# Optimization experiments

Measured on AMD Instinct MI355X. Metric: run time of the kernel, lower is better.

Reference implementation:

```python
import jax, jax.numpy as jnp
import numpy as np

B, T, I, H, O = 64, 1024, 64, 512, 24


def _gru_cell(x, h, w_ih, w_hh, b_ih, b_hh):
    # PyTorch GRUCell math. w_ih: [3H, in], w_hh: [3H, H]
    gi = x @ w_ih.T + b_ih   # [B, 3H]
    gh = h @ w_hh.T + b_hh   # [B, 3H]
    i_r, i_z, i_n = jnp.split(gi, 3, axis=-1)
    h_r, h_z, h_n = jnp.split(gh, 3, axis=-1)
    r = jax.nn.sigmoid(i_r + h_r)
    z = jax.nn.sigmoid(i_z + h_z)
    n = jnp.tanh(i_n + r * h_n)
    return (1.0 - z) * n + z * h


def setup_inputs() -> dict:
    key = jax.random.key(0)
    ks = jax.random.split(key, 13)
    s1 = 1.0 / np.sqrt(H)
    u = lambda k, shape: jax.random.uniform(k, shape, jnp.float32, -s1, s1)
    return {
        "x": jax.random.normal(ks[0], (B, T, I), jnp.float32),
        "w_ih1": u(ks[1], (3 * H, I)),
        "w_hh1": u(ks[2], (3 * H, H)),
        "b_ih1": u(ks[3], (3 * H,)),
        "b_hh1": u(ks[4], (3 * H,)),
        "w_ih2": u(ks[5], (3 * H, H)),
        "w_hh2": u(ks[6], (3 * H, H)),
        "b_ih2": u(ks[7], (3 * H,)),
        "b_hh2": u(ks[8], (3 * H,)),
        "w_o1": u(ks[9], (O, H)),
        "b_o1": u(ks[10], (O,)),
        "w_o2": u(ks[11], (O, H)),
        "b_o2": u(ks[12], (O,)),
    }


def reference(x, w_ih1, w_hh1, b_ih1, b_hh1, w_ih2, w_hh2, b_ih2, b_hh2,
              w_o1, b_o1, w_o2, b_o2):
    batch = x.shape[0]
    h0 = jnp.zeros((batch, H), x.dtype)

    def step(carry, x_t):
        h1, h2 = carry
        h1 = _gru_cell(x_t, h1, w_ih1, w_hh1, b_ih1, b_hh1)
        h2 = _gru_cell(h1, h2, w_ih2, w_hh2, b_ih2, b_hh2)
        out = jnp.tanh(h1 @ w_o1.T + b_o1) + jnp.tanh(h2 @ w_o2.T + b_o2)
        return (h1, h2), out

    xs = jnp.transpose(x, (1, 0, 2))  # [T, B, I]
    _, outs = jax.lax.scan(step, (h0, h0), xs)  # outs: [T, B, O]
    return jnp.transpose(outs, (1, 0, 2))  # [B, T, O]
```

## Files before the change

kernel.cpp:

```cpp
#include <hip/hip_runtime.h>

typedef unsigned short u16;
typedef unsigned int u32;
typedef unsigned long long u64;
typedef __attribute__((ext_vector_type(8))) short bf16x8;
typedef __attribute__((ext_vector_type(4))) float f32x4;
typedef __attribute__((ext_vector_type(4))) u32 u32x4;

namespace {
constexpr int kT = 1024, kI = 64, kH = 512, kO = 24;
constexpr int kBH = 64 * kH;
constexpr int kNWG = 100;
constexpr unsigned kBarOff = 16u * (unsigned)kBH * 2u;
}

__device__ __forceinline__ u16 f2bf(float f) {
  union { float f; u32 u; } c; c.f = f;
  u32 u = c.u + 0x7FFFu + ((c.u >> 16) & 1u);
  return (u16)(u >> 16);
}
__device__ __forceinline__ float sigf(float x) { return 1.0f / (1.0f + __expf(-x)); }
__device__ __forceinline__ float tanhf_(float x) {
  float e = __expf(2.0f * x); return 1.0f - 2.0f / (e + 1.0f);
}
__device__ __forceinline__ bf16x8 cvt8(const float* p) {
  const float4 f0 = *reinterpret_cast<const float4*>(p);
  const float4 f1 = *reinterpret_cast<const float4*>(p + 4);
  bf16x8 r;
  r[0] = (short)f2bf(f0.x); r[1] = (short)f2bf(f0.y);
  r[2] = (short)f2bf(f0.z); r[3] = (short)f2bf(f0.w);
  r[4] = (short)f2bf(f1.x); r[5] = (short)f2bf(f1.y);
  r[6] = (short)f2bf(f1.z); r[7] = (short)f2bf(f1.w);
  return r;
}
__device__ __forceinline__ f32x4 mfma(bf16x8 a, bf16x8 b, f32x4 c) {
  return __builtin_amdgcn_mfma_f32_16x16x32_bf16(a, b, c, 0, 0, 0);
}
__device__ __forceinline__ int ldflag(const int* s, int i) {
  return __hip_atomic_load(&s[i], __ATOMIC_RELAXED, __HIP_MEMORY_SCOPE_AGENT);
}
__device__ __forceinline__ void stflag(int* s, int i, int v) {
  __hip_atomic_store(&s[i], v, __ATOMIC_RELAXED, __HIP_MEMORY_SCOPE_AGENT);
}
__device__ __forceinline__ void barrier_lds() {
  asm volatile("s_waitcnt lgkmcnt(0)" ::: "memory");
  __builtin_amdgcn_s_barrier();
}
union V16 { u32x4 u; bf16x8 v; };
__device__ __forceinline__ void fetch4(const u16* p, bf16x8* ch) {
  u32x4 a, b, c, d;
  asm volatile(
    "global_load_dwordx4 %0, %4, off sc0 sc1\n\t"
    "global_load_dwordx4 %1, %4, off offset:64 sc0 sc1\n\t"
    "global_load_dwordx4 %2, %4, off offset:128 sc0 sc1\n\t"
    "global_load_dwordx4 %3, %4, off offset:192 sc0 sc1\n\t"
    "s_waitcnt vmcnt(0)"
    : "=&v"(a), "=&v"(b), "=&v"(c), "=&v"(d) : "v"(p) : "memory");
  V16 t;
  t.u = a; ch[0] = t.v;  t.u = b; ch[1] = t.v;
  t.u = c; ch[2] = t.v;  t.u = d; ch[3] = t.v;
}
__device__ __forceinline__ void fetch8(const u16* p, bf16x8* ch) {
  u32x4 a, b, c, d, e, f, g2, h;
  asm volatile(
    "global_load_dwordx4 %0, %8, off sc0 sc1\n\t"
    "global_load_dwordx4 %1, %8, off offset:64 sc0 sc1\n\t"
    "global_load_dwordx4 %2, %8, off offset:128 sc0 sc1\n\t"
    "global_load_dwordx4 %3, %8, off offset:192 sc0 sc1\n\t"
    "global_load_dwordx4 %4, %8, off offset:256 sc0 sc1\n\t"
    "global_load_dwordx4 %5, %8, off offset:320 sc0 sc1\n\t"
    "global_load_dwordx4 %6, %8, off offset:384 sc0 sc1\n\t"
    "global_load_dwordx4 %7, %8, off offset:448 sc0 sc1\n\t"
    "s_waitcnt vmcnt(0)"
    : "=&v"(a), "=&v"(b), "=&v"(c), "=&v"(d),
      "=&v"(e), "=&v"(f), "=&v"(g2), "=&v"(h) : "v"(p) : "memory");
  V16 t;
  t.u = a; ch[0] = t.v;  t.u = b;  ch[1] = t.v;
  t.u = c; ch[2] = t.v;  t.u = d;  ch[3] = t.v;
  t.u = e; ch[4] = t.v;  t.u = f;  ch[5] = t.v;
  t.u = g2; ch[6] = t.v; t.u = h;  ch[7] = t.v;
}
__device__ __forceinline__ u32 pat3(int t3) {
  return ((u32)t3 & 1u) | ((((u32)t3 >> 1) & 1u) << 16);
}
template<int N>
__device__ __forceinline__ bool tagsok(const bf16x8* ch, u32 pat) {
  bool ok = true;
#pragma unroll
  for (int c = 0; c < N; ++c) {
    union { bf16x8 v; u32 u[4]; } t; t.v = ch[c];
    ok = ok && ((t.u[0] & 0x10001u) == pat) && ((t.u[2] & 0x10001u) == pat);
  }
  return ok;
}
template<int N>
__device__ __forceinline__ void dataD(const u16* p, u32 pat, bf16x8* ch) {
  int spins = 0;
  for (;;) {
    u64 g0 = __hip_atomic_load((const u64*)p, __ATOMIC_RELAXED, __HIP_MEMORY_SCOPE_AGENT);
    if (__all(((u32)g0 & 0x10001u) == pat)) break;
    if ((++spins & 3) == 3) __builtin_amdgcn_s_sleep(1);
  }
  spins = 0;
  for (;;) {
    if constexpr (N == 4) fetch4(p, ch); else fetch8(p, ch);
    if (__all(tagsok<N>(ch, pat))) break;
    if ((++spins & 7) == 7) __builtin_amdgcn_s_sleep(1);
  }
  __asm__ volatile("" ::: "memory");
}
template<int N>
__device__ __forceinline__ void dataO(const u16* p, u32 pat, bf16x8* ch) {
  if constexpr (N == 4) fetch4(p, ch); else fetch8(p, ch);
  if (__all(tagsok<N>(ch, pat))) { __asm__ volatile("" ::: "memory"); return; }
  int spins = 0;
  for (;;) {
    u64 g0 = __hip_atomic_load((const u64*)p, __ATOMIC_RELAXED, __HIP_MEMORY_SCOPE_AGENT);
    if (__all(((u32)g0 & 0x10001u) == pat)) break;
    if ((++spins & 3) == 3) __builtin_amdgcn_s_sleep(1);
  }
  spins = 0;
  for (;;) {
    if constexpr (N == 4) fetch4(p, ch); else fetch8(p, ch);
    if (__all(tagsok<N>(ch, pat))) break;
    if ((++spins & 7) == 7) __builtin_amdgcn_s_sleep(1);
  }
  __asm__ volatile("" ::: "memory");
}
__device__ __forceinline__ void st_h(u16* p, const float* h, int t3) {
  u16 a = (u16)((f2bf(h[0]) & ~1u) | ((u32)t3 & 1u));
  u16 b = (u16)((f2bf(h[1]) & ~1u) | (((u32)t3 >> 1) & 1u));
  u64 v = (u64)a | ((u64)b << 16) | ((u64)f2bf(h[2]) << 32) | ((u64)f2bf(h[3]) << 48);
  __hip_atomic_store((u64*)p, v, __ATOMIC_RELAXED, __HIP_MEMORY_SCOPE_AGENT);
}
__device__ __forceinline__ void throttle8(const int* f, int idx, bool act,
                                          int k, int& bound) {
  if (bound >= k - 7) return;
  for (;;) {
    int v = act ? ldflag(f, idx) : 0x7fffffff;
    if (__all(v >= k - 7)) {
      bound = __all(v >= k - 1) ? (k - 1) : (__all(v >= k - 4) ? (k - 4) : (k - 7));
      break;
    }
    __builtin_amdgcn_s_sleep(2);
  }
}

__global__ __launch_bounds__(256, 1) void stackgru(
    const float* __restrict__ x,
    const float* __restrict__ wih1, const float* __restrict__ whh1,
    const float* __restrict__ bih1, const float* __restrict__ bhh1,
    const float* __restrict__ wih2, const float* __restrict__ whh2,
    const float* __restrict__ bih2, const float* __restrict__ bhh2,
    const float* __restrict__ wo1, const float* __restrict__ bo1,
    const float* __restrict__ wo2, const float* __restrict__ bo2,
    float* __restrict__ out, u16* __restrict__ hbuf, int* __restrict__ ctl)
{
  __shared__ float red[4][3][4][64][4];
  __shared__ float redx[2][4][64][4];
  __shared__ float sbias[4][64];
  const int wg = blockIdx.x;
  const int tid = threadIdx.x;
  const int lane = tid & 63;
  const int w = tid >> 6;
  const int l15 = lane & 15;
  const int q = lane >> 4;

  u16* h1b = hbuf;
  u16* h2b = hbuf + 8 * kBH;

  if (wg < 32) {
    const int ub = wg >> 2, g = wg & 3;
    const int U0 = ub * 64;
    const int bb = g * 16 + l15;
    const int kh = w;
    bf16x8 whf[3][4][4];
#pragma unroll
    for (int gg = 0; gg < 3; ++gg)
#pragma unroll
      for (int m = 0; m < 4; ++m)
#pragma unroll
        for (int c = 0; c < 4; ++c)
          whf[gg][m][c] = cvt8(whh1 + (size_t)(gg * kH + U0 + m * 16 + l15) * kH
                               + (kh * 4 + c) * 32 + q * 8);
    const bool hasx = (kh == 1 || kh == 2);
    const int xch = kh - 1;
    bf16x8 aihf[3][4];
    if (hasx)
#pragma unroll
      for (int gg = 0; gg < 3; ++gg)
#pragma unroll
        for (int m = 0; m < 4; ++m)
          aihf[gg][m] = cvt8(wih1 + (size_t)(gg * kH + U0 + m * 16 + l15) * kI
                             + xch * 32 + q * 8);
    if (tid < 64) {
      int u = U0 + tid;
      sbias[0][tid] = bih1[u]          + bhh1[u];
      sbias[1][tid] = bih1[kH + u]     + bhh1[kH + u];
      sbias[2][tid] = bih1[2 * kH + u];
      sbias[3][tid] = bhh1[2 * kH + u];
    }
    float h1l[4];
#pragma unroll
    for (int r = 0; r < 4; ++r) h1l[r] = 0.0f;
    __syncthreads();
    const int thridx = (lane < 16) ? (lane * 4 + g) : (64 + g);
    const bool thract = (lane < 17);
    int bound = 0;
    for (int k = 1; k <= kT; ++k) {
      const int t3 = k % 3, t3p = (k - 1) % 3;
      bf16x8 xf;
      if (hasx)
        xf = cvt8(x + ((size_t)bb * kT + (k - 1)) * kI + xch * 32 + q * 8);
      bf16x8 ch[4];
      dataO<4>(h1b + ((k - 1) & 7) * kBH + (size_t)bb * kH + kh * 128 + q * 8,
               pat3(t3p), ch);
      f32x4 aR[4], aZ[4], aN[4];
#pragma unroll
      for (int m = 0; m < 4; ++m) { aR[m] = {0,0,0,0}; aZ[m] = {0,0,0,0}; aN[m] = {0,0,0,0}; }
#pragma unroll
      for (int m = 0; m < 4; ++m)
#pragma unroll
        for (int c = 0; c < 4; ++c) {
          aR[m] = mfma(whf[0][m][c], ch[c], aR[m]);
          aZ[m] = mfma(whf[1][m][c], ch[c], aZ[m]);
          aN[m] = mfma(whf[2][m][c], ch[c], aN[m]);
        }
      if (hasx) {
        f32x4 xN[4];
#pragma unroll
        for (int m = 0; m < 4; ++m) xN[m] = {0,0,0,0};
#pragma unroll
        for (int m = 0; m < 4; ++m) {
          aR[m] = mfma(aihf[0][m], xf, aR[m]);
          aZ[m] = mfma(aihf[1][m], xf, aZ[m]);
          xN[m] = mfma(aihf[2][m], xf, xN[m]);
        }
#pragma unroll
        for (int m = 0; m < 4; ++m)
#pragma unroll
          for (int r = 0; r < 4; ++r) redx[xch][m][lane][r] = xN[m][r];
      }
#pragma unroll
      for (int m = 0; m < 4; ++m)
#pragma unroll
        for (int r = 0; r < 4; ++r) {
          red[kh][0][m][lane][r] = aR[m][r];
          red[kh][1][m][lane][r] = aZ[m][r];
          red[kh][2][m][lane][r] = aN[m][r];
        }
      if (kh == 0) throttle8(ctl, thridx, thract, k, bound);
      __syncthreads();
      {
        float hnew[4];
#pragma unroll
        for (int r = 0; r < 4; ++r) {
          float sR = red[0][0][w][lane][r] + red[1][0][w][lane][r]
                   + red[2][0][w][lane][r] + red[3][0][w][lane][r];
          float sZ = red[0][1][w][lane][r] + red[1][1][w][lane][r]
                   + red[2][1][w][lane][r] + red[3][1][w][lane][r];
          float sN = red[0][2][w][lane][r] + red[1][2][w][lane][r]
                   + red[2][2][w][lane][r] + red[3][2][w][lane][r];
          float sNi = redx[0][w][lane][r] + redx[1][w][lane][r];
          int uu = w * 16 + q * 4 + r;
          float rr = sigf(sR + sbias[0][uu]);
          float zz = sigf(sZ + sbias[1][uu]);
          float nn = tanhf_(sNi + sbias[2][uu] + rr * (sN + sbias[3][uu]));
          float h  = (1.0f - zz) * nn + zz * h1l[r];
          h1l[r] = h; hnew[r] = h;
        }
        st_h(h1b + (k & 7) * kBH + (size_t)bb * kH + U0 + w * 16 + q * 4, hnew, t3);
      }
      barrier_lds();
    }
  } else if (wg < 96) {
    const int j2 = wg - 32;
    const int ub2 = j2 >> 2, g = j2 & 3;
    const int U0 = ub2 * 32;
    const int bb = g * 16 + l15;
    const int kh = w;
    const float* src = (kh < 2) ? wih2 : whh2;
    const int koff = (kh & 1) * 256;
    bf16x8 whf[3][2][8];
#pragma unroll
    for (int gg = 0; gg < 3; ++gg)
#pragma unroll
      for (int m = 0; m < 2; ++m)
#pragma unroll
        for (int c = 0; c < 8; ++c)
          whf[gg][m][c] = cvt8(src + (size_t)(gg * kH + U0 + m * 16 + l15) * kH
                               + koff + c * 32 + q * 8);
    if (tid < 32) {
      int u = U0 + tid;
      sbias[0][tid] = bih2[u]          + bhh2[u];
      sbias[1][tid] = bih2[kH + u]     + bhh2[kH + u];
      sbias[2][tid] = bih2[2 * kH + u];
      sbias[3][tid] = bhh2[2 * kH + u];
    }
    float h2l[4];
#pragma unroll
    for (int r = 0; r < 4; ++r) h2l[r] = 0.0f;
    __syncthreads();
    int bound = 0;
    for (int k = 1; k <= kT; ++k) {
      const int t3 = k % 3, t3p = (k - 1) % 3;
      bf16x8 ch[8];
      if (kh < 2) {
        dataD<8>(h1b + (k & 7) * kBH + (size_t)bb * kH + koff + q * 8,
                 pat3(t3), ch);
      } else {
        dataO<8>(h2b + ((k - 1) & 7) * kBH + (size_t)bb * kH + koff + q * 8,
                 pat3(t3p), ch);
      }
      f32x4 a[3][2];
#pragma unroll
      for (int gg = 0; gg < 3; ++gg)
#pragma unroll
        for (int m = 0; m < 2; ++m) a[gg][m] = {0,0,0,0};
#pragma unroll
      for (int m = 0; m < 2; ++m)
#pragma unroll
        for (int c = 0; c < 8; ++c) {
          a[0][m] = mfma(whf[0][m][c], ch[c], a[0][m]);
          a[1][m] = mfma(whf[1][m][c], ch[c], a[1][m]);
          a[2][m] = mfma(whf[2][m][c], ch[c], a[2][m]);
        }
#pragma unroll
      for (int gg = 0; gg < 3; ++gg)
#pragma unroll
        for (int m = 0; m < 2; ++m)
#pragma unroll
          for (int r = 0; r < 4; ++r) red[kh][gg][m][lane][r] = a[gg][m][r];
      if (kh == 0) throttle8(ctl, 64 + g, lane < 1, k, bound);
      __syncthreads();
      if (tid == 0) stflag(ctl, j2, k);
      if (w < 2) {
        const int m = w;
        float hnew[4];
#pragma unroll
        for (int r = 0; r < 4; ++r) {
          float gi0 = red[0][0][m][lane][r] + red[1][0][m][lane][r];
          float gi1 = red[0][1][m][lane][r] + red[1][1][m][lane][r];
          float gi2 = red[0][2][m][lane][r] + red[1][2][m][lane][r];
          float gh0 = red[2][0][m][lane][r] + red[3][0][m][lane][r];
          float gh1 = red[2][1][m][lane][r] + red[3][1][m][lane][r];
          float gh2 = red[2][2][m][lane][r] + red[3][2][m][lane][r];
          int uu = m * 16 + q * 4 + r;
          float rr = sigf(gi0 + gh0 + sbias[0][uu]);
          float zz = sigf(gi1 + gh1 + sbias[1][uu]);
          float nn = tanhf_(gi2 + sbias[2][uu] + rr * (gh2 + sbias[3][uu]));
          float h  = (1.0f - zz) * nn + zz * h2l[r];
          h2l[r] = h; hnew[r] = h;
        }
        st_h(h2b + (k & 7) * kBH + (size_t)bb * kH + U0 + m * 16 + q * 4, hnew, t3);
      }
      barrier_lds();
    }
  } else {
    const int g3 = wg - 96;
    const int bb = g3 * 16 + l15;
    const int mat = w & 1, khh = w >> 1;
    const float* wsel = mat ? wo2 : wo1;
    bf16x8 zf = {0,0,0,0,0,0,0,0};
    bf16x8 wof[2][8];
#pragma unroll
    for (int t = 0; t < 2; ++t)
#pragma unroll
      for (int c = 0; c < 8; ++c) {
        int row = t * 16 + l15;
        wof[t][c] = (row < kO) ? cvt8(wsel + (size_t)row * kH + khh * 256 + c * 32 + q * 8) : zf;
      }
    float bv1[2][4], bv2[2][4];
#pragma unroll
    for (int t = 0; t < 2; ++t)
#pragma unroll
      for (int r = 0; r < 4; ++r) {
        int o = t * 16 + q * 4 + r;
        bv1[t][r] = (o < kO) ? bo1[o] : 0.0f;
        bv2[t][r] = (o < kO) ? bo2[o] : 0.0f;
      }
    const bool fin = (mat == 0 && khh == 0);
    const u16* slab = mat ? h2b : h1b;
    for (int k = 1; k <= kT; ++k) {
      const u32 pat = pat3(k % 3);
      bf16x8 ch[8];
      dataD<8>(slab + (k & 7) * kBH + (size_t)bb * kH + khh * 256 + q * 8, pat, ch);
      f32x4 a0 = {0,0,0,0}, a1 = {0,0,0,0};
#pragma unroll
      for (int c = 0; c < 8; ++c) {
        a0 = mfma(wof[0][c], ch[c], a0);
        a1 = mfma(wof[1][c], ch[c], a1);
      }
      if (!fin) {
        const int s = mat * 2 + khh - 1;
#pragma unroll
        for (int r = 0; r < 4; ++r) {
          red[s][0][0][lane][r] = a0[r];
          red[s][0][1][lane][r] = a1[r];
        }
      }
      __syncthreads();
      if (tid == 0) stflag(ctl, 64 + g3, k);
      if (fin) {
#pragma unroll
        for (int t = 0; t < 2; ++t) {
          int o0 = t * 16 + q * 4;
          if (o0 < kO) {
            f32x4 av = (t == 0) ? a0 : a1;
            float4 ov;
            ov.x = tanhf_(av[0] + red[0][0][t][lane][0] + bv1[t][0]) +
                   tanhf_(red[1][0][t][lane][0] + red[2][0][t][lane][0] + bv2[t][0]);
            ov.y = tanhf_(av[1] + red[0][0][t][lane][1] + bv1[t][1]) +
                   tanhf_(red[1][0][t][lane][1] + red[2][0][t][lane][1] + bv2[t][1]);
            ov.z = tanhf_(av[2] + red[0][0][t][lane][2] + bv1[t][2]) +
                   tanhf_(red[1][0][t][lane][2] + red[2][0][t][lane][2] + bv2[t][2]);
            ov.w = tanhf_(av[3] + red[0][0][t][lane][3] + bv1[t][3]) +
                   tanhf_(red[1][0][t][lane][3] + red[2][0][t][lane][3] + bv2[t][3]);
            *reinterpret_cast<float4*>(out + ((size_t)bb * kT + (k - 1)) * kO + o0) = ov;
          }
        }
      }
      barrier_lds();
    }
  }
}

extern "C" void kernel_launch(void* const* d_in, const int* in_sizes, int n_in,
                              void* d_out, int out_size, void* d_ws, size_t ws_size,
                              hipStream_t stream) {
  (void)in_sizes; (void)n_in; (void)out_size; (void)ws_size;
  hipMemsetAsync(d_ws, 0, kBarOff + 1024, stream);
  hipMemsetAsync((char*)d_ws + 3u * kBH * 2u, 0x01, kBH * 2u, stream);
  hipMemsetAsync((char*)d_ws + 6u * kBH * 2u, 0x01, kBH * 2u, stream);
  hipMemsetAsync((char*)d_ws + (8u + 3u) * kBH * 2u, 0x01, kBH * 2u, stream);
  hipMemsetAsync((char*)d_ws + (8u + 6u) * kBH * 2u, 0x01, kBH * 2u, stream);
  const float* x    = (const float*)d_in[0];
  const float* wih1 = (const float*)d_in[1];
  const float* whh1 = (const float*)d_in[2];
  const float* bih1 = (const float*)d_in[3];
  const float* bhh1 = (const float*)d_in[4];
  const float* wih2 = (const float*)d_in[5];
  const float* whh2 = (const float*)d_in[6];
  const float* bih2 = (const float*)d_in[7];
  const float* bhh2 = (const float*)d_in[8];
  const float* wo1  = (const float*)d_in[9];
  const float* bo1  = (const float*)d_in[10];
  const float* wo2  = (const float*)d_in[11];
  const float* bo2  = (const float*)d_in[12];
  float* out  = (float*)d_out;
  u16* hbuf   = (u16*)d_ws;
  int* ctl    = (int*)((char*)d_ws + kBarOff);
  stackgru<<<dim3(kNWG), dim3(256), 0, stream>>>(
      x, wih1, whh1, bih1, bhh1, wih2, whh2, bih2, bhh2,
      wo1, bo1, wo2, bo2, out, hbuf, ctl);
}
```

Baseline: 4.259 ms.

## Halve workgroup count by processing two batch groups per workgroup per step

Each workgroup now handles two 16-row batch groups serially within every timestep, reusing its register-resident weight fragments, so the persistent grid shrinks from 100 to 50 workgroups. The goal is fewer participants in the cross-workgroup flag and throttle synchronisation and less total weight-loading setup. In exchange, each workgroup does twice the serial work per step, with two LDS reductions and two barriers, which lengthens the critical path of the recurrence.

```diff
diff --git a/kernel.cpp b/kernel.cpp
--- a/kernel.cpp
+++ b/kernel.cpp
@@ -10,7 +10,7 @@
 namespace {
 constexpr int kT = 1024, kI = 64, kH = 512, kO = 24;
 constexpr int kBH = 64 * kH;
-constexpr int kNWG = 100;
+constexpr int kNWG = 50;
 constexpr unsigned kBarOff = 16u * (unsigned)kBH * 2u;
 }
 
@@ -169,10 +169,9 @@
   u16* h1b = hbuf;
   u16* h2b = hbuf + 8 * kBH;
 
-  if (wg < 32) {
-    const int ub = wg >> 2, g = wg & 3;
+  if (wg < 16) {
+    const int ub = wg >> 1, gp = wg & 1;
     const int U0 = ub * 64;
-    const int bb = g * 16 + l15;
     const int kh = w;
     bf16x8 whf[3][4][4];
 #pragma unroll
@@ -200,84 +199,90 @@
       sbias[2][tid] = bih1[2 * kH + u];
       sbias[3][tid] = bhh1[2 * kH + u];
     }
-    float h1l[4];
-#pragma unroll
-    for (int r = 0; r < 4; ++r) h1l[r] = 0.0f;
+    float h1l[2][4];
+#pragma unroll
+    for (int s = 0; s < 2; ++s)
+#pragma unroll
+      for (int r = 0; r < 4; ++r) h1l[s][r] = 0.0f;
+    int bnd[2] = {0, 0};
     __syncthreads();
-    const int thridx = (lane < 16) ? (lane * 4 + g) : (64 + g);
-    const bool thract = (lane < 17);
-    int bound = 0;
     for (int k = 1; k <= kT; ++k) {
       const int t3 = k % 3, t3p = (k - 1) % 3;
-      bf16x8 xf;
-      if (hasx)
-        xf = cvt8(x + ((size_t)bb * kT + (k - 1)) * kI + xch * 32 + q * 8);
-      bf16x8 ch[4];
-      dataO<4>(h1b + ((k - 1) & 7) * kBH + (size_t)bb * kH + kh * 128 + q * 8,
-               pat3(t3p), ch);
-      f32x4 aR[4], aZ[4], aN[4];
-#pragma unroll
-      for (int m = 0; m < 4; ++m) { aR[m] = {0,0,0,0}; aZ[m] = {0,0,0,0}; aN[m] = {0,0,0,0}; }
-#pragma unroll
-      for (int m = 0; m < 4; ++m)
-#pragma unroll
-        for (int c = 0; c < 4; ++c) {
-          aR[m] = mfma(whf[0][m][c], ch[c], aR[m]);
-          aZ[m] = mfma(whf[1][m][c], ch[c], aZ[m]);
-          aN[m] = mfma(whf[2][m][c], ch[c], aN[m]);
-        }
-      if (hasx) {
-        f32x4 xN[4];
-#pragma unroll
-        for (int m = 0; m < 4; ++m) xN[m] = {0,0,0,0};
-#pragma unroll
-        for (int m = 0; m < 4; ++m) {
-          aR[m] = mfma(aihf[0][m], xf, aR[m]);
-          aZ[m] = mfma(aihf[1][m], xf, aZ[m]);
-          xN[m] = mfma(aihf[2][m], xf, xN[m]);
-        }
+#pragma unroll
+      for (int s = 0; s < 2; ++s) {
+        const int g = gp * 2 + s;
+        const int bb = g * 16 + l15;
+        const int thridx = (lane < 16) ? (lane * 4 + g) : (64 + g);
+        const bool thract = (lane < 17);
+        bf16x8 xf;
+        if (hasx)
+          xf = cvt8(x + ((size_t)bb * kT + (k - 1)) * kI + xch * 32 + q * 8);
+        bf16x8 ch[4];
+        dataO<4>(h1b + ((k - 1) & 7) * kBH + (size_t)bb * kH + kh * 128 + q * 8,
+                 pat3(t3p), ch);
+        f32x4 aR[4], aZ[4], aN[4];
+#pragma unroll
+        for (int m = 0; m < 4; ++m) { aR[m] = {0,0,0,0}; aZ[m] = {0,0,0,0}; aN[m] = {0,0,0,0}; }
 #pragma unroll
         for (int m = 0; m < 4; ++m)
 #pragma unroll
-          for (int r = 0; r < 4; ++r) redx[xch][m][lane][r] = xN[m][r];
+          for (int c = 0; c < 4; ++c) {
+            aR[m] = mfma(whf[0][m][c], ch[c], aR[m]);
+            aZ[m] = mfma(whf[1][m][c], ch[c], aZ[m]);
+            aN[m] = mfma(whf[2][m][c], ch[c], aN[m]);
+          }
+        if (hasx) {
+          f32x4 xN[4];
+#pragma unroll
+          for (int m = 0; m < 4; ++m) xN[m] = {0,0,0,0};
+#pragma unroll
+          for (int m = 0; m < 4; ++m) {
+            aR[m] = mfma(aihf[0][m], xf, aR[m]);
+            aZ[m] = mfma(aihf[1][m], xf, aZ[m]);
+            xN[m] = mfma(aihf[2][m], xf, xN[m]);
+          }
+#pragma unroll
+          for (int m = 0; m < 4; ++m)
+#pragma unroll
+            for (int r = 0; r < 4; ++r) redx[xch][m][lane][r] = xN[m][r];
+        }
+#pragma unroll
+        for (int m = 0; m < 4; ++m)
+#pragma unroll
+          for (int r = 0; r < 4; ++r) {
+            red[kh][0][m][lane][r] = aR[m][r];
+            red[kh][1][m][lane][r] = aZ[m][r];
+            red[kh][2][m][lane][r] = aN[m][r];
+          }
+        if (kh == 0) throttle8(ctl, thridx, thract, k, bnd[s]);
+        __syncthreads();
+        {
+          float hnew[4];
+#pragma unroll
+          for (int r = 0; r < 4; ++r) {
+            float sR = red[0][0][w][lane][r] + red[1][0][w][lane][r]
+                     + red[2][0][w][lane][r] + red[3][0][w][lane][r];
+            float sZ = red[0][1][w][lane][r] + red[1][1][w][lane][r]
+                     + red[2][1][w][lane][r] + red[3][1][w][lane][r];
+            float sN = red[0][2][w][lane][r] + red[1][2][w][lane][r]
+                     + red[2][2][w][lane][r] + red[3][2][w][lane][r];
+            float sNi = redx[0][w][lane][r] + redx[1][w][lane][r];
+            int uu = w * 16 + q * 4 + r;
+            float rr = sigf(sR + sbias[0][uu]);
+            float zz = sigf(sZ + sbias[1][uu]);
+            float nn = tanhf_(sNi + sbias[2][uu] + rr * (sN + sbias[3][uu]));
+            float h  = (1.0f - zz) * nn + zz * h1l[s][r];
+            h1l[s][r] = h; hnew[r] = h;
+          }
+          st_h(h1b + (k & 7) * kBH + (size_t)bb * kH + U0 + w * 16 + q * 4, hnew, t3);
+        }
+        barrier_lds();
       }
-#pragma unroll
-      for (int m = 0; m < 4; ++m)
-#pragma unroll
-        for (int r = 0; r < 4; ++r) {
-          red[kh][0][m][lane][r] = aR[m][r];
-          red[kh][1][m][lane][r] = aZ[m][r];
-          red[kh][2][m][lane][r] = aN[m][r];
-        }
-      if (kh == 0) throttle8(ctl, thridx, thract, k, bound);
-      __syncthreads();
-      {
-        float hnew[4];
-#pragma unroll
-        for (int r = 0; r < 4; ++r) {
-          float sR = red[0][0][w][lane][r] + red[1][0][w][lane][r]
-                   + red[2][0][w][lane][r] + red[3][0][w][lane][r];
-          float sZ = red[0][1][w][lane][r] + red[1][1][w][lane][r]
-                   + red[2][1][w][lane][r] + red[3][1][w][lane][r];
-          float sN = red[0][2][w][lane][r] + red[1][2][w][lane][r]
-                   + red[2][2][w][lane][r] + red[3][2][w][lane][r];
-          float sNi = redx[0][w][lane][r] + redx[1][w][lane][r];
-          int uu = w * 16 + q * 4 + r;
-          float rr = sigf(sR + sbias[0][uu]);
-          float zz = sigf(sZ + sbias[1][uu]);
-          float nn = tanhf_(sNi + sbias[2][uu] + rr * (sN + sbias[3][uu]));
-          float h  = (1.0f - zz) * nn + zz * h1l[r];
-          h1l[r] = h; hnew[r] = h;
-        }
-        st_h(h1b + (k & 7) * kBH + (size_t)bb * kH + U0 + w * 16 + q * 4, hnew, t3);
-      }
-      barrier_lds();
-    }
-  } else if (wg < 96) {
-    const int j2 = wg - 32;
-    const int ub2 = j2 >> 2, g = j2 & 3;
+    }
+  } else if (wg < 48) {
+    const int j2 = wg - 16;
+    const int ub2 = j2 >> 1, gp = j2 & 1;
     const int U0 = ub2 * 32;
-    const int bb = g * 16 + l15;
     const int kh = w;
     const float* src = (kh < 2) ? wih2 : whh2;
     const int koff = (kh & 1) * 256;
@@ -297,68 +302,74 @@
       sbias[2][tid] = bih2[2 * kH + u];
       sbias[3][tid] = bhh2[2 * kH + u];
     }
-    float h2l[4];
-#pragma unroll
-    for (int r = 0; r < 4; ++r) h2l[r] = 0.0f;
+    float h2l[2][4];
+#pragma unroll
+    for (int s = 0; s < 2; ++s)
+#pragma unroll
+      for (int r = 0; r < 4; ++r) h2l[s][r] = 0.0f;
+    int bnd[2] = {0, 0};
     __syncthreads();
-    int bound = 0;
     for (int k = 1; k <= kT; ++k) {
       const int t3 = k % 3, t3p = (k - 1) % 3;
-      bf16x8 ch[8];
-      if (kh < 2) {
-        dataD<8>(h1b + (k & 7) * kBH + (size_t)bb * kH + koff + q * 8,
-                 pat3(t3), ch);
-      } else {
-        dataO<8>(h2b + ((k - 1) & 7) * kBH + (size_t)bb * kH + koff + q * 8,
-                 pat3(t3p), ch);
+#pragma unroll
+      for (int s = 0; s < 2; ++s) {
+        const int g = gp * 2 + s;
+        const int bb = g * 16 + l15;
+        bf16x8 ch[8];
+        if (kh < 2) {
+          dataD<8>(h1b + (k & 7) * kBH + (size_t)bb * kH + koff + q * 8,
+                   pat3(t3), ch);
+        } else {
+          dataO<8>(h2b + ((k - 1) & 7) * kBH + (size_t)bb * kH + koff + q * 8,
+                   pat3(t3p), ch);
+        }
+        f32x4 a[3][2];
+#pragma unroll
+        for (int gg = 0; gg < 3; ++gg)
+#pragma unroll
+          for (int m = 0; m < 2; ++m) a[gg][m] = {0,0,0,0};
+#pragma unroll
+        for (int m = 0; m < 2; ++m)
+#pragma unroll
+          for (int c = 0; c < 8; ++c) {
+            a[0][m] = mfma(whf[0][m][c], ch[c], a[0][m]);
+            a[1][m] = mfma(whf[1][m][c], ch[c], a[1][m]);
+            a[2][m] = mfma(whf[2][m][c], ch[c], a[2][m]);
+          }
+#pragma unroll
+        for (int gg = 0; gg < 3; ++gg)
+#pragma unroll
+          for (int m = 0; m < 2; ++m)
+#pragma unroll
+            for (int r = 0; r < 4; ++r) red[kh][gg][m][lane][r] = a[gg][m][r];
+        if (kh == 0) throttle8(ctl, 64 + g, lane < 1, k, bnd[s]);
+        __syncthreads();
+        if (tid == 0) stflag(ctl, ub2 * 4 + g, k);
+        if (w < 2) {
+          const int m = w;
+          float hnew[4];
+#pragma unroll
+          for (int r = 0; r < 4; ++r) {
+            float gi0 = red[0][0][m][lane][r] + red[1][0][m][lane][r];
+            float gi1 = red[0][1][m][lane][r] + red[1][1][m][lane][r];
+            float gi2 = red[0][2][m][lane][r] + red[1][2][m][lane][r];
+            float gh0 = red[2][0][m][lane][r] + red[3][0][m][lane][r];
+            float gh1 = red[2][1][m][lane][r] + red[3][1][m][lane][r];
+            float gh2 = red[2][2][m][lane][r] + red[3][2][m][lane][r];
+            int uu = m * 16 + q * 4 + r;
+            float rr = sigf(gi0 + gh0 + sbias[0][uu]);
+            float zz = sigf(gi1 + gh1 + sbias[1][uu]);
+            float nn = tanhf_(gi2 + sbias[2][uu] + rr * (gh2 + sbias[3][uu]));
+            float h  = (1.0f - zz) * nn + zz * h2l[s][r];
+            h2l[s][r] = h; hnew[r] = h;
+          }
+          st_h(h2b + (k & 7) * kBH + (size_t)bb * kH + U0 + m * 16 + q * 4, hnew, t3);
+        }
+        barrier_lds();
       }
-      f32x4 a[3][2];
-#pragma unroll
-      for (int gg = 0; gg < 3; ++gg)
-#pragma unroll
-        for (int m = 0; m < 2; ++m) a[gg][m] = {0,0,0,0};
-#pragma unroll
-      for (int m = 0; m < 2; ++m)
-#pragma unroll
-        for (int c = 0; c < 8; ++c) {
-          a[0][m] = mfma(whf[0][m][c], ch[c], a[0][m]);
-          a[1][m] = mfma(whf[1][m][c], ch[c], a[1][m]);
-          a[2][m] = mfma(whf[2][m][c], ch[c], a[2][m]);
-        }
-#pragma unroll
-      for (int gg = 0; gg < 3; ++gg)
-#pragma unroll
-        for (int m = 0; m < 2; ++m)
-#pragma unroll
-          for (int r = 0; r < 4; ++r) red[kh][gg][m][lane][r] = a[gg][m][r];
-      if (kh == 0) throttle8(ctl, 64 + g, lane < 1, k, bound);
-      __syncthreads();
-      if (tid == 0) stflag(ctl, j2, k);
-      if (w < 2) {
-        const int m = w;
-        float hnew[4];
-#pragma unroll
-        for (int r = 0; r < 4; ++r) {
-          float gi0 = red[0][0][m][lane][r] + red[1][0][m][lane][r];
-          float gi1 = red[0][1][m][lane][r] + red[1][1][m][lane][r];
-          float gi2 = red[0][2][m][lane][r] + red[1][2][m][lane][r];
-          float gh0 = red[2][0][m][lane][r] + red[3][0][m][lane][r];
-          float gh1 = red[2][1][m][lane][r] + red[3][1][m][lane][r];
-          float gh2 = red[2][2][m][lane][r] + red[3][2][m][lane][r];
-          int uu = m * 16 + q * 4 + r;
-          float rr = sigf(gi0 + gh0 + sbias[0][uu]);
-          float zz = sigf(gi1 + gh1 + sbias[1][uu]);
-          float nn = tanhf_(gi2 + sbias[2][uu] + rr * (gh2 + sbias[3][uu]));
-          float h  = (1.0f - zz) * nn + zz * h2l[r];
-          h2l[r] = h; hnew[r] = h;
-        }
-        st_h(h2b + (k & 7) * kBH + (size_t)bb * kH + U0 + m * 16 + q * 4, hnew, t3);
-      }
-      barrier_lds();
     }
   } else {
-    const int g3 = wg - 96;
-    const int bb = g3 * 16 + l15;
+    const int gp = wg - 48;
     const int mat = w & 1, khh = w >> 1;
     const float* wsel = mat ? wo2 : wo1;
     bf16x8 zf = {0,0,0,0,0,0,0,0};
@@ -383,44 +394,49 @@
     const u16* slab = mat ? h2b : h1b;
     for (int k = 1; k <= kT; ++k) {
       const u32 pat = pat3(k % 3);
-      bf16x8 ch[8];
-      dataD<8>(slab + (k & 7) * kBH + (size_t)bb * kH + khh * 256 + q * 8, pat, ch);
-      f32x4 a0 = {0,0,0,0}, a1 = {0,0,0,0};
-#pragma unroll
-      for (int c = 0; c < 8; ++c) {
-        a0 = mfma(wof[0][c], ch[c], a0);
-        a1 = mfma(wof[1][c], ch[c], a1);
+#pragma unroll
+      for (int s = 0; s < 2; ++s) {
+        const int g = gp * 2 + s;
+        const int bb = g * 16 + l15;
+        bf16x8 ch[8];
+        dataD<8>(slab + (k & 7) * kBH + (size_t)bb * kH + khh * 256 + q * 8, pat, ch);
+        f32x4 a0 = {0,0,0,0}, a1 = {0,0,0,0};
+#pragma unroll
+        for (int c = 0; c < 8; ++c) {
+          a0 = mfma(wof[0][c], ch[c], a0);
+          a1 = mfma(wof[1][c], ch[c], a1);
+        }
+        if (!fin) {
+          const int sl = mat * 2 + khh - 1;
+#pragma unroll
+          for (int r = 0; r < 4; ++r) {
+            red[sl][0][0][lane][r] = a0[r];
+            red[sl][0][1][lane][r] = a1[r];
+          }
+        }
+        __syncthreads();
+        if (tid == 0) stflag(ctl, 64 + g, k);
+        if (fin) {
+#pragma unroll
+          for (int t = 0; t < 2; ++t) {
+            int o0 = t * 16 + q * 4;
+            if (o0 < kO) {
+              f32x4 av = (t == 0) ? a0 : a1;
+              float4 ov;
+              ov.x = tanhf_(av[0] + red[0][0][t][lane][0] + bv1[t][0]) +
+                     tanhf_(red[1][0][t][lane][0] + red[2][0][t][lane][0] + bv2[t][0]);
+              ov.y = tanhf_(av[1] + red[0][0][t][lane][1] + bv1[t][1]) +
+                     tanhf_(red[1][0][t][lane][1] + red[2][0][t][lane][1] + bv2[t][1]);
+              ov.z = tanhf_(av[2] + red[0][0][t][lane][2] + bv1[t][2]) +
+                     tanhf_(red[1][0][t][lane][2] + red[2][0][t][lane][2] + bv2[t][2]);
+              ov.w = tanhf_(av[3] + red[0][0][t][lane][3] + bv1[t][3]) +
+                     tanhf_(red[1][0][t][lane][3] + red[2][0][t][lane][3] + bv2[t][3]);
+              *reinterpret_cast<float4*>(out + ((size_t)bb * kT + (k - 1)) * kO + o0) = ov;
+            }
+          }
+        }
+        barrier_lds();
       }
-      if (!fin) {
-        const int s = mat * 2 + khh - 1;
-#pragma unroll
-        for (int r = 0; r < 4; ++r) {
-          red[s][0][0][lane][r] = a0[r];
-          red[s][0][1][lane][r] = a1[r];
-        }
-      }
-      __syncthreads();
-      if (tid == 0) stflag(ctl, 64 + g3, k);
-      if (fin) {
-#pragma unroll
-        for (int t = 0; t < 2; ++t) {
-          int o0 = t * 16 + q * 4;
-          if (o0 < kO) {
-            f32x4 av = (t == 0) ? a0 : a1;
-            float4 ov;
-            ov.x = tanhf_(av[0] + red[0][0][t][lane][0] + bv1[t][0]) +
-                   tanhf_(red[1][0][t][lane][0] + red[2][0][t][lane][0] + bv2[t][0]);
-            ov.y = tanhf_(av[1] + red[0][0][t][lane][1] + bv1[t][1]) +
-                   tanhf_(red[1][0][t][lane][1] + red[2][0][t][lane][1] + bv2[t][1]);
-            ov.z = tanhf_(av[2] + red[0][0][t][lane][2] + bv1[t][2]) +
-                   tanhf_(red[1][0][t][lane][2] + red[2][0][t][lane][2] + bv2[t][2]);
-            ov.w = tanhf_(av[3] + red[0][0][t][lane][3] + bv1[t][3]) +
-                   tanhf_(red[1][0][t][lane][3] + red[2][0][t][lane][3] + bv2[t][3]);
-            *reinterpret_cast<float4*>(out + ((size_t)bb * kT + (k - 1)) * kO + o0) = ov;
-          }
-        }
-      }
-      barrier_lds();
     }
   }
 }
```

After: 5.998 ms. +40.9%, slower.
